# Performance work log

Measured on AMD Instinct MI355X. Metric: run time of the kernel, lower is better.

## Reference

```python
import jax, jax.numpy as jnp
import numpy as np

B, S, H = 2, 1024, 768
D, HID = 24, 96            # hdim_proj_dim, hdim_mlp_hidden
VIN, VHID = 3 * H, 2 * max(128, H // 2)  # concat_hadam -> 3H; out_hid = 768
ALPHA0 = 0.05              # init_gate_hdim


def setup_inputs() -> dict:
    key = jax.random.key(0)
    ks = jax.random.split(key, 10)
    sc = 0.02
    return {
        "H_j": jax.random.normal(ks[0], (B, S, H), jnp.float32),
        "H_i": jax.random.normal(ks[1], (B, S, H), jnp.float32),
        "attn_mask": jnp.ones((B, S), jnp.float32),
        "Wpj": jax.random.normal(ks[2], (H, D), jnp.float32) * sc,
        "Wpi": jax.random.normal(ks[3], (H, D), jnp.float32) * sc,
        "W1": jax.random.normal(ks[4], (4 * D, HID), jnp.float32) * sc,
        "b1": jnp.zeros((HID,), jnp.float32),
        "W2": jax.random.normal(ks[5], (HID, 1), jnp.float32) * sc,
        "b2": jnp.zeros((1,), jnp.float32),
        "Wv1": jax.random.normal(ks[6], (VIN, VHID), jnp.float32) * sc,
        "bv1": jnp.zeros((VHID,), jnp.float32),
        "Wv2": jax.random.normal(ks[7], (VHID, H), jnp.float32) * sc,
        "bv2": jnp.zeros((H,), jnp.float32),
        "alpha": jnp.float32(ALPHA0),
    }


def reference(H_j, H_i, attn_mask, Wpj, Wpi, W1, b1, W2, b2, Wv1, bv1, Wv2, bv2, alpha):
    # token projections: [B,S,D]
    Zj = H_j @ Wpj
    Zi = H_i @ Wpi
    # 4-term pair MLP, decomposed so the [B,S,S,4D] concat is never built:
    # cat([Zj_pair, Zi_pair, Zj*Zi, |Zj-Zi|]) @ W1 == sum of 4 partial products
    W1a, W1b, W1c, W1d = W1[:D], W1[D:2 * D], W1[2 * D:3 * D], W1[3 * D:]
    tj = Zj @ W1a                                   # [B,S,HID]
    ti = Zi @ W1b                                   # [B,S,HID]
    had = jnp.einsum('bsd,btd,dh->bsth', Zj, Zi, W1c)          # [B,S,S,HID]
    diff = jnp.abs(Zj[:, :, None, :] - Zi[:, None, :, :]) @ W1d  # [B,S,S,HID]
    h = jax.nn.relu(tj[:, :, None, :] + ti[:, None, :, :] + had + diff + b1)
    logits = (h @ W2)[..., 0] + b2[0]               # [B,S,S]
    # additive mask on key axis (torch: (1-mask)*finfo.min)
    logits = logits + (1.0 - attn_mask[:, None, :]) * jnp.finfo(logits.dtype).min
    probs = jax.nn.softmax(logits, axis=-1)
    ctx = jnp.einsum('bst,bth->bsh', probs, H_i)    # context over H_i
    # value fusion: concat_hadam -> [ctx, H_j, ctx*H_j]
    msg_in = jnp.concatenate([ctx, H_j, ctx * H_j], axis=-1)
    msg = jax.nn.relu(msg_in @ Wv1 + bv1) @ Wv2 + bv2
    return alpha * msg  # dropout is identity at eval
```

## Files before the change

kernel.cpp:

```cpp
#include <hip/hip_runtime.h>
#include <math.h>

#define BB   2
#define SS   1024
#define HH   768
#define DD   24
#define HIDD 96
#define VINN 2304
#define VHIDD 768
#define NRR  2048

typedef __attribute__((ext_vector_type(8))) short short8;
typedef __attribute__((ext_vector_type(4))) float floatx4;

static __device__ inline unsigned short f2bf(float x) {
    unsigned int u = __float_as_uint(x);
    u = (u + 0x7FFFu + ((u >> 16) & 1u)) >> 16;
    return (unsigned short)u;
}
static __device__ inline unsigned int pack2(float a, float b) {
    return (unsigned int)f2bf(a) | ((unsigned int)f2bf(b) << 16);
}

static __device__ inline void gl16(const unsigned short* g, unsigned short* l) {
    __builtin_amdgcn_global_load_lds(
        (const __attribute__((address_space(1))) unsigned int*)g,
        (__attribute__((address_space(3))) unsigned int*)l,
        16, 0, 0);
}

__global__ __launch_bounds__(256) void k_tconv(
    const float* __restrict__ in, unsigned short* __restrict__ out,
    int R, int C)
{
    size_t zoff = (size_t)blockIdx.z * R * C;
    in += zoff; out += zoff;
    __shared__ float tile[32][33];
    int r0 = blockIdx.y * 32, c0 = blockIdx.x * 32;
    int tc = threadIdx.x & 31, tr = threadIdx.x >> 5;
    #pragma unroll
    for (int i = 0; i < 4; ++i)
        tile[tr + i*8][tc] = in[(size_t)(r0 + tr + i*8)*C + c0 + tc];
    __syncthreads();
    #pragma unroll
    for (int i = 0; i < 4; ++i)
        out[(size_t)(c0 + tr + i*8)*R + r0 + tc] = f2bf(tile[tc][tr + i*8]);
}

__global__ __launch_bounds__(256) void k_zproj(
    const float* __restrict__ Hj, const float* __restrict__ Hi,
    const float* __restrict__ Wpj, const float* __restrict__ Wpi,
    unsigned* __restrict__ Zjp, unsigned* __restrict__ Zip)
{
    __shared__ __align__(16) unsigned short sA[64][72];
    __shared__ __align__(16) unsigned short sBT[32][72];
    int tid = threadIdx.x;
    int w = tid >> 6, lane = tid & 63;
    int quad = lane >> 4, col = lane & 15;

    int m0 = blockIdx.x * 64;
    bool isJ = (m0 < NRR);
    const float* src = isJ ? Hj : Hi;
    const float* Wp  = isJ ? Wpj : Wpi;
    unsigned* Zp     = isJ ? Zjp : Zip;
    int rowbase = isJ ? m0 : (m0 - NRR);

    floatx4 acc[2];
    acc[0] = (floatx4){0.f,0.f,0.f,0.f};
    acc[1] = (floatx4){0.f,0.f,0.f,0.f};

    for (int kb = 0; kb < HH; kb += 64) {
        #pragma unroll
        for (int i = 0; i < 4; ++i) {
            int f4 = tid + i*256;
            int r = f4 >> 4, c4 = f4 & 15;
            float4 v = *(const float4*)(src + (size_t)(rowbase + r)*HH + kb + c4*4);
            uint2 pkt; pkt.x = pack2(v.x, v.y); pkt.y = pack2(v.z, v.w);
            *(uint2*)&sA[r][c4*4] = pkt;
        }
        {
            const float* wsrc = Wp + (size_t)kb*DD;
            #pragma unroll
            for (int i = 0; i < 6; ++i) {
                int idx = tid + i*256;
                int k = idx / DD, n = idx % DD;
                sBT[n][k] = f2bf(wsrc[idx]);
            }
        }
        __syncthreads();
        #pragma unroll
        for (int kt = 0; kt < 2; ++kt) {
            short8 av = *(const short8*)&sA[w*16 + col][kt*32 + quad*8];
            #pragma unroll
            for (int nt = 0; nt < 2; ++nt) {
                short8 bv = *(const short8*)&sBT[nt*16 + col][kt*32 + quad*8];
                acc[nt] = __builtin_amdgcn_mfma_f32_16x16x32_bf16(av, bv, acc[nt], 0, 0, 0);
            }
        }
        __syncthreads();
    }
    #pragma unroll
    for (int nt = 0; nt < 2; ++nt) {
        #pragma unroll
        for (int r = 0; r < 4; ++r) {
            float v = acc[nt][r];
            float vn = __shfl_xor(v, 1, 64);
            int n = nt*16 + col;
            if (!(col & 1) && n < DD) {
                int m = w*16 + quad*4 + r;
                Zp[(size_t)(rowbase + m)*12 + (n >> 1)] = pack2(v, vn);
            }
        }
    }
}

#define LSTR 72
#define TC 128
__global__ __launch_bounds__(256) void k_attn(
    const unsigned* __restrict__ Zjp, const unsigned* __restrict__ Zip,
    const float* __restrict__ W1, const float* __restrict__ b1,
    const float* __restrict__ W2,
    const float* __restrict__ mask, unsigned short* __restrict__ probs)
{
    int row = blockIdx.x;
    int b = row >> 10;
    int tid = threadIdx.x;
    int lane = tid & 63, wv = tid >> 6;
    int quad = lane >> 4, col = lane & 15;

    __shared__ __align__(16) unsigned short sAB[2][TC*LSTR];
    __shared__ __align__(16) float sLog[SS];
    __shared__ unsigned sZjp[12];
    __shared__ float sW2[HIDD];
    __shared__ float sRed[4];

    if (tid < 12) sZjp[tid] = Zjp[(size_t)row*12 + tid];
    if (tid < HIDD) sW2[tid] = W2[tid];
    __syncthreads();

    if (tid < HIDD) {
        int h = tid;
        float zj[24];
        #pragma unroll
        for (int u = 0; u < 12; ++u) {
            unsigned z = sZjp[u];
            zj[2*u]   = __uint_as_float(z << 16);
            zj[2*u+1] = __uint_as_float(z & 0xffff0000u);
        }
        float tj = b1[h];
        #pragma unroll
        for (int d = 0; d < DD; ++d) tj = fmaf(zj[d], W1[d*HIDD + h], tj);
        unsigned short* rowp = &sAB[0][h*LSTR];
        #pragma unroll
        for (int d = 0; d < DD; ++d)
            rowp[d] = f2bf(fmaf(zj[d], W1[(48+d)*HIDD + h], W1[(24+d)*HIDD + h]));
        #pragma unroll
        for (int d = 0; d < DD; ++d)
            rowp[24+d] = f2bf(W1[(72+d)*HIDD + h]);
        rowp[48] = f2bf(tj);
        #pragma unroll
        for (int k = 49; k < 64; ++k) rowp[k] = 0;
    }
    __syncthreads();

    short8 bfr[6][2];
    #pragma unroll
    for (int nf = 0; nf < 6; ++nf)
        #pragma unroll
        for (int kt = 0; kt < 2; ++kt)
            bfr[nf][kt] = *(const short8*)&sAB[0][(nf*16 + col)*LSTR + kt*32 + quad*8];
    float4 w2q[6];
    #pragma unroll
    for (int nf = 0; nf < 6; ++nf)
        w2q[nf] = *(const float4*)&sW2[nf*16 + quad*4];
    __syncthreads();

    {
        int r = tid >> 1, bf = tid & 1;
        unsigned short* rowp = &sAB[bf][r*LSTR];
        uint4 w0; w0.x = 0x3F80u; w0.y = 0; w0.z = 0; w0.w = 0;
        *(uint4*)&rowp[48] = w0;
        uint4 zz; zz.x = 0; zz.y = 0; zz.z = 0; zz.w = 0;
        *(uint4*)&rowp[56] = zz;
    }

    int t_loc = tid >> 1, hh = tid & 1;
    const unsigned* zbase = Zip + (size_t)(b << 10) * 12;

    auto pack = [&](int chunk, int bf) {
        int t = chunk*TC + t_loc;
        const unsigned* zr = zbase + (size_t)t*12;
        unsigned short* rowp = &sAB[bf][t_loc*LSTR];
        uint4 first = *(const uint4*)(zr + hh*4);
        *(uint4*)&rowp[hh*8] = first;
        uint2 ext; ext.x = 0; ext.y = 0;
        if (hh) {
            uint4 second = *(const uint4*)(zr + 8);
            *(uint4*)&rowp[16] = second;
            unsigned myz[6] = {first.z, first.w, second.x, second.y, second.z, second.w};
            unsigned q[6];
            #pragma unroll
            for (int u = 0; u < 6; ++u) {
                unsigned za = sZjp[6 + u], zb = myz[u];
                float alo = __uint_as_float(za << 16);
                float ahi = __uint_as_float(za & 0xffff0000u);
                float blo = __uint_as_float(zb << 16);
                float bhi = __uint_as_float(zb & 0xffff0000u);
                unsigned dlo = __float_as_uint(fabsf(alo - blo)) + 0x8000u;
                unsigned dhi = __float_as_uint(fabsf(ahi - bhi)) + 0x8000u;
                q[u] = __builtin_amdgcn_perm(dhi, dlo, 0x07060302u);
            }
            #pragma unroll
            for (int j = 0; j < 3; ++j) {
                uint2 wq; wq.x = q[2*j]; wq.y = q[2*j+1];
                *(uint2*)&rowp[36 + 4*j] = wq;
            }
        } else {
            ext = *(const uint2*)(zr + 4);
            unsigned myz[6] = {first.x, first.y, first.z, first.w, ext.x, ext.y};
            unsigned q[6];
            #pragma unroll
            for (int u = 0; u < 6; ++u) {
                unsigned za = sZjp[u], zb = myz[u];
                float alo = __uint_as_float(za << 16);
                float ahi = __uint_as_float(za & 0xffff0000u);
                float blo = __uint_as_float(zb << 16);
                float bhi = __uint_as_float(zb & 0xffff0000u);
                unsigned dlo = __float_as_uint(fabsf(alo - blo)) + 0x8000u;
                unsigned dhi = __float_as_uint(fabsf(ahi - bhi)) + 0x8000u;
                q[u] = __builtin_amdgcn_perm(dhi, dlo, 0x07060302u);
            }
            #pragma unroll
            for (int j = 0; j < 3; ++j) {
                uint2 wq; wq.x = q[2*j]; wq.y = q[2*j+1];
                *(uint2*)&rowp[24 + 4*j] = wq;
            }
        }
    };

    pack(0, 0);
    __syncthreads();

    for (int chunk = 0; chunk < SS/TC; ++chunk) {
        int cur = chunk & 1;
        if (chunk + 1 < SS/TC) pack(chunk + 1, cur ^ 1);

        short8 av[2][2];
        #pragma unroll
        for (int tt = 0; tt < 2; ++tt) {
            int arow = (wv*2 + tt)*16 + col;
            av[tt][0] = *(const short8*)&sAB[cur][arow*LSTR + quad*8];
            av[tt][1] = *(const short8*)&sAB[cur][arow*LSTR + 32 + quad*8];
        }
        float s0 = 0.f, s1 = 0.f;
        #pragma unroll
        for (int hf = 0; hf < 6; ++hf) {
            floatx4 a0 = {0.f,0.f,0.f,0.f}, a1 = {0.f,0.f,0.f,0.f};
            a0 = __builtin_amdgcn_mfma_f32_16x16x32_bf16(bfr[hf][0], av[0][0], a0, 0, 0, 0);
            a0 = __builtin_amdgcn_mfma_f32_16x16x32_bf16(bfr[hf][1], av[0][1], a0, 0, 0, 0);
            a1 = __builtin_amdgcn_mfma_f32_16x16x32_bf16(bfr[hf][0], av[1][0], a1, 0, 0, 0);
            a1 = __builtin_amdgcn_mfma_f32_16x16x32_bf16(bfr[hf][1], av[1][1], a1, 0, 0, 0);
            float w2v[4] = {w2q[hf].x, w2q[hf].y, w2q[hf].z, w2q[hf].w};
            #pragma unroll
            for (int r = 0; r < 4; ++r) {
                s0 = fmaf(fmaxf(a0[r], 0.f), w2v[r], s0);
                s1 = fmaf(fmaxf(a1[r], 0.f), w2v[r], s1);
            }
        }
        s0 += __shfl_xor(s0, 16, 64);  s0 += __shfl_xor(s0, 32, 64);
        s1 += __shfl_xor(s1, 16, 64);  s1 += __shfl_xor(s1, 32, 64);
        if (lane < 16) {
            sLog[chunk*TC + (wv*2 + 0)*16 + lane] = s0;
            sLog[chunk*TC + (wv*2 + 1)*16 + lane] = s1;
        }
        __syncthreads();
    }

    float lv[4];
    #pragma unroll
    for (int i = 0; i < 4; ++i) {
        int t = tid + i*256;
        lv[i] = sLog[t] + (1.0f - mask[(size_t)(b<<10) + t]) * (-3.402823466e+38f);
    }
    float m = fmaxf(fmaxf(lv[0], lv[1]), fmaxf(lv[2], lv[3]));
    #pragma unroll
    for (int off = 32; off; off >>= 1) m = fmaxf(m, __shfl_down(m, off, 64));
    if (lane == 0) sRed[wv] = m;
    __syncthreads();
    float M = fmaxf(fmaxf(sRed[0], sRed[1]), fmaxf(sRed[2], sRed[3]));
    float e[4]; float ssum = 0.f;
    #pragma unroll
    for (int i = 0; i < 4; ++i) { e[i] = expf(lv[i] - M); ssum += e[i]; }
    #pragma unroll
    for (int off = 32; off; off >>= 1) ssum += __shfl_down(ssum, off, 64);
    __syncthreads();
    if (lane == 0) sRed[wv] = ssum;
    __syncthreads();
    float inv = 1.0f / (sRed[0] + sRed[1] + sRed[2] + sRed[3]);
    #pragma unroll
    for (int i = 0; i < 4; ++i)
        probs[(size_t)row*SS + tid + i*256] = f2bf(e[i] * inv);
}

__global__ __launch_bounds__(256) void k_mgemm_p(
    const unsigned short* __restrict__ A,
    const unsigned short* __restrict__ BT,
    float* __restrict__ P,
    int K, int bt_bstride)
{
    __shared__ __align__(16) unsigned short sA[64*64];
    __shared__ __align__(16) unsigned short sB[64*64];
    int tid = threadIdx.x;
    int w = tid >> 6, lane = tid & 63;
    int quad = lane >> 4, col = lane & 15;

    int n0 = blockIdx.x * 64, m0 = blockIdx.y * 64;
    int z = blockIdx.z;
    int kslice = K >> 1;
    int k0 = z * kslice;
    int nk = kslice >> 6;
    const unsigned short* Bb = BT + (size_t)(m0 >> 10) * bt_bstride;

    int srow = lane >> 3;
    int skc  = (lane & 7) * 8;

    floatx4 acc[4];
    #pragma unroll
    for (int nf = 0; nf < 4; ++nf) acc[nf] = (floatx4){0.f,0.f,0.f,0.f};

    for (int kb = 0; kb < nk; ++kb) {
        int kofs = k0 + kb*64;
        #pragma unroll
        for (int i = 0; i < 2; ++i) {
            int rbase = w*16 + i*8;
            gl16(A  + (size_t)(m0 + rbase + srow)*K + kofs + skc, &sA[rbase*64]);
            gl16(Bb + (size_t)(n0 + rbase + srow)*K + kofs + skc, &sB[rbase*64]);
        }
        __syncthreads();
        #pragma unroll
        for (int kt = 0; kt < 2; ++kt) {
            short8 av = *(const short8*)&sA[(w*16 + col)*64 + kt*32 + quad*8];
            #pragma unroll
            for (int nf = 0; nf < 4; ++nf) {
                short8 bv = *(const short8*)&sB[(nf*16 + col)*64 + kt*32 + quad*8];
                acc[nf] = __builtin_amdgcn_mfma_f32_16x16x32_bf16(av, bv, acc[nf], 0, 0, 0);
            }
        }
        __syncthreads();
    }

    float* Pz = P + (size_t)z*NRR*768;
    #pragma unroll
    for (int nf = 0; nf < 4; ++nf) {
        int n = n0 + nf*16 + col;
        #pragma unroll
        for (int r = 0; r < 4; ++r) {
            int m = w*16 + quad*4 + r;
            Pz[(size_t)(m0 + m)*768 + n] = acc[nf][r];
        }
    }
}

template<int MODE>
__global__ __launch_bounds__(256) void k_epi(
    const float* __restrict__ P,
    const float* __restrict__ bias,
    const float* __restrict__ Hj,
    const float* __restrict__ alpha_p,
    void* __restrict__ Cout)
{
    int idx = blockIdx.x*256 + threadIdx.x;
    int g = idx / 192, c = (idx % 192) * 4;
    float4 v0 = *(const float4*)(P + (size_t)g*768 + c);
    float4 v1 = *(const float4*)(P + (size_t)NRR*768 + (size_t)g*768 + c);
    float v[4] = {v0.x+v1.x, v0.y+v1.y, v0.z+v1.z, v0.w+v1.w};
    if (MODE == 0) {
        float4 h4 = *(const float4*)(Hj + (size_t)g*HH + c);
        float hj[4] = {h4.x, h4.y, h4.z, h4.w};
        unsigned short* msgin = (unsigned short*)Cout;
        uint2 wc, wh, wp;
        wc.x = pack2(v[0], v[1]);        wc.y = pack2(v[2], v[3]);
        wh.x = pack2(hj[0], hj[1]);      wh.y = pack2(hj[2], hj[3]);
        wp.x = pack2(v[0]*hj[0], v[1]*hj[1]);
        wp.y = pack2(v[2]*hj[2], v[3]*hj[3]);
        *(uint2*)&msgin[(size_t)g*VINN + c]        = wc;
        *(uint2*)&msgin[(size_t)g*VINN + HH + c]   = wh;
        *(uint2*)&msgin[(size_t)g*VINN + 2*HH + c] = wp;
    } else if (MODE == 1) {
        float4 b4 = *(const float4*)(bias + c);
        uint2 wy;
        wy.x = pack2(fmaxf(v[0]+b4.x, 0.f), fmaxf(v[1]+b4.y, 0.f));
        wy.y = pack2(fmaxf(v[2]+b4.z, 0.f), fmaxf(v[3]+b4.w, 0.f));
        *(uint2*)&((unsigned short*)Cout)[(size_t)g*VHIDD + c] = wy;
    } else {
        float a = alpha_p[0];
        float4 b4 = *(const float4*)(bias + c);
        float4 o;
        o.x = a*(v[0]+b4.x); o.y = a*(v[1]+b4.y);
        o.z = a*(v[2]+b4.z); o.w = a*(v[3]+b4.w);
        *(float4*)&((float*)Cout)[(size_t)g*HH + c] = o;
    }
}

extern "C" void kernel_launch(void* const* d_in, const int* in_sizes, int n_in,
                              void* d_out, int out_size, void* d_ws, size_t ws_size,
                              hipStream_t stream)
{
    const float* Hj   = (const float*)d_in[0];
    const float* Hi   = (const float*)d_in[1];
    const float* mask = (const float*)d_in[2];
    const float* Wpj  = (const float*)d_in[3];
    const float* Wpi  = (const float*)d_in[4];
    const float* W1   = (const float*)d_in[5];
    const float* b1   = (const float*)d_in[6];
    const float* W2   = (const float*)d_in[7];
    const float* Wv1  = (const float*)d_in[9];
    const float* bv1  = (const float*)d_in[10];
    const float* Wv2  = (const float*)d_in[11];
    const float* bv2  = (const float*)d_in[12];
    const float* alpha = (const float*)d_in[13];
    float* out = (float*)d_out;

    const int NR = NRR;
    char* p = (char*)d_ws;
    auto alloc = [&](size_t bytes) {
        char* r = p; p += (bytes + 255) & ~(size_t)255; return r;
    };
    unsigned* Zjp          = (unsigned*)alloc((size_t)NR*12*4);
    unsigned* Zip          = (unsigned*)alloc((size_t)NR*12*4);
    unsigned short* probsb = (unsigned short*)alloc((size_t)NR*SS*2);
    unsigned short* HiT    = (unsigned short*)alloc((size_t)BB*HH*SS*2);
    unsigned short* Wv1T   = (unsigned short*)alloc((size_t)VHIDD*VINN*2);
    unsigned short* Wv2T   = (unsigned short*)alloc((size_t)HH*VHIDD*2);
    unsigned short* msginb = (unsigned short*)alloc((size_t)NR*VINN*2);
    unsigned short* Y1b    = (unsigned short*)alloc((size_t)NR*VHIDD*2);
    float* Part            = (float*)alloc((size_t)2*NR*768*4);

    k_tconv<<<dim3(VHIDD/32, VINN/32, 1), 256, 0, stream>>>(Wv1, Wv1T, VINN, VHIDD);
    k_tconv<<<dim3(HH/32, VHIDD/32, 1), 256, 0, stream>>>(Wv2, Wv2T, VHIDD, HH);
    k_tconv<<<dim3(HH/32, SS/32, BB), 256, 0, stream>>>(Hi, HiT, SS, HH);
    k_zproj<<<2*NR/64, 256, 0, stream>>>(Hj, Hi, Wpj, Wpi, Zjp, Zip);
    k_attn<<<NR, 256, 0, stream>>>(Zjp, Zip, W1, b1, W2, mask, probsb);

    const int EPI_GRID = NR*192/256;

    k_mgemm_p<<<dim3(HH/64, NR/64, 2), 256, 0, stream>>>(
        probsb, HiT, Part, SS, HH*SS);
    k_epi<0><<<EPI_GRID, 256, 0, stream>>>(Part, nullptr, Hj, alpha, msginb);

    k_mgemm_p<<<dim3(VHIDD/64, NR/64, 2), 256, 0, stream>>>(
        msginb, Wv1T, Part, VINN, 0);
    k_epi<1><<<EPI_GRID, 256, 0, stream>>>(Part, bv1, nullptr, alpha, Y1b);

    k_mgemm_p<<<dim3(HH/64, NR/64, 2), 256, 0, stream>>>(
        Y1b, Wv2T, Part, VHIDD, 0);
    k_epi<2><<<EPI_GRID, 256, 0, stream>>>(Part, bv2, nullptr, alpha, out);
}
```

Before: 216.9 us.

## Merge prep kernels and fuse epilogues into non-split-K GEMMs

```diff
diff --git a/kernel.cpp b/kernel.cpp
--- a/kernel.cpp
+++ b/kernel.cpp
@@ -29,15 +29,97 @@
         16, 0, 0);
 }
 
-__global__ __launch_bounds__(256) void k_tconv(
-    const float* __restrict__ in, unsigned short* __restrict__ out,
-    int R, int C)
+__global__ __launch_bounds__(256) void k_prep(
+    const float* __restrict__ Hj, const float* __restrict__ Hi,
+    const float* __restrict__ Wpj, const float* __restrict__ Wpi,
+    const float* __restrict__ Wv1, const float* __restrict__ Wv2,
+    unsigned* __restrict__ Zjp, unsigned* __restrict__ Zip,
+    unsigned short* __restrict__ Wv1T, unsigned short* __restrict__ Wv2T,
+    unsigned short* __restrict__ HiT)
 {
-    size_t zoff = (size_t)blockIdx.z * R * C;
-    in += zoff; out += zoff;
+    __shared__ __align__(16) unsigned short sAz[64][72];
+    __shared__ __align__(16) unsigned short sBTz[32][72];
     __shared__ float tile[32][33];
-    int r0 = blockIdx.y * 32, c0 = blockIdx.x * 32;
-    int tc = threadIdx.x & 31, tr = threadIdx.x >> 5;
+    int bid = blockIdx.x;
+    int tid = threadIdx.x;
+
+    if (bid < 64) {
+        int w = tid >> 6, lane = tid & 63;
+        int quad = lane >> 4, col = lane & 15;
+        int m0 = bid * 64;
+        bool isJ = (m0 < NRR);
+        const float* src = isJ ? Hj : Hi;
+        const float* Wp  = isJ ? Wpj : Wpi;
+        unsigned* Zp     = isJ ? Zjp : Zip;
+        int rowbase = isJ ? m0 : (m0 - NRR);
+
+        floatx4 acc[2];
+        acc[0] = (floatx4){0.f,0.f,0.f,0.f};
+        acc[1] = (floatx4){0.f,0.f,0.f,0.f};
+
+        for (int kb = 0; kb < HH; kb += 64) {
+            #pragma unroll
+            for (int i = 0; i < 4; ++i) {
+                int f4 = tid + i*256;
+                int r = f4 >> 4, c4 = f4 & 15;
+                float4 v = *(const float4*)(src + (size_t)(rowbase + r)*HH + kb + c4*4);
+                uint2 pkt; pkt.x = pack2(v.x, v.y); pkt.y = pack2(v.z, v.w);
+                *(uint2*)&sAz[r][c4*4] = pkt;
+            }
+            {
+                const float* wsrc = Wp + (size_t)kb*DD;
+                #pragma unroll
+                for (int i = 0; i < 6; ++i) {
+                    int idx = tid + i*256;
+                    int k = idx / DD, n = idx % DD;
+                    sBTz[n][k] = f2bf(wsrc[idx]);
+                }
+            }
+            __syncthreads();
+            #pragma unroll
+            for (int kt = 0; kt < 2; ++kt) {
+                short8 av = *(const short8*)&sAz[w*16 + col][kt*32 + quad*8];
+                #pragma unroll
+                for (int nt = 0; nt < 2; ++nt) {
+                    short8 bv = *(const short8*)&sBTz[nt*16 + col][kt*32 + quad*8];
+                    acc[nt] = __builtin_amdgcn_mfma_f32_16x16x32_bf16(av, bv, acc[nt], 0, 0, 0);
+                }
+            }
+            __syncthreads();
+        }
+        #pragma unroll
+        for (int nt = 0; nt < 2; ++nt) {
+            #pragma unroll
+            for (int r = 0; r < 4; ++r) {
+                float v = acc[nt][r];
+                float vn = __shfl_xor(v, 1, 64);
+                int n = nt*16 + col;
+                if (!(col & 1) && n < DD) {
+                    int m = w*16 + quad*4 + r;
+                    Zp[(size_t)(rowbase + m)*12 + (n >> 1)] = pack2(v, vn);
+                }
+            }
+        }
+        return;
+    }
+
+    int b2 = bid - 64;
+    const float* in; unsigned short* out; int R, C, r0, c0;
+    if (b2 < 1728) {
+        in = Wv1; out = Wv1T; R = VINN; C = VHIDD;
+        c0 = (b2 % 24) * 32; r0 = (b2 / 24) * 32;
+    } else if (b2 < 2304) {
+        int t = b2 - 1728;
+        in = Wv2; out = Wv2T; R = VHIDD; C = HH;
+        c0 = (t % 24) * 32; r0 = (t / 24) * 32;
+    } else {
+        int t = b2 - 2304;
+        int z = t / 768; t %= 768;
+        in = Hi + (size_t)z*SS*HH; out = HiT + (size_t)z*HH*SS;
+        R = SS; C = HH;
+        c0 = (t % 24) * 32; r0 = (t / 24) * 32;
+    }
+    int tc = tid & 31, tr = tid >> 5;
     #pragma unroll
     for (int i = 0; i < 4; ++i)
         tile[tr + i*8][tc] = in[(size_t)(r0 + tr + i*8)*C + c0 + tc];
@@ -45,73 +127,6 @@
     #pragma unroll
     for (int i = 0; i < 4; ++i)
         out[(size_t)(c0 + tr + i*8)*R + r0 + tc] = f2bf(tile[tc][tr + i*8]);
-}
-
-__global__ __launch_bounds__(256) void k_zproj(
-    const float* __restrict__ Hj, const float* __restrict__ Hi,
-    const float* __restrict__ Wpj, const float* __restrict__ Wpi,
-    unsigned* __restrict__ Zjp, unsigned* __restrict__ Zip)
-{
-    __shared__ __align__(16) unsigned short sA[64][72];
-    __shared__ __align__(16) unsigned short sBT[32][72];
-    int tid = threadIdx.x;
-    int w = tid >> 6, lane = tid & 63;
-    int quad = lane >> 4, col = lane & 15;
-
-    int m0 = blockIdx.x * 64;
-    bool isJ = (m0 < NRR);
-    const float* src = isJ ? Hj : Hi;
-    const float* Wp  = isJ ? Wpj : Wpi;
-    unsigned* Zp     = isJ ? Zjp : Zip;
-    int rowbase = isJ ? m0 : (m0 - NRR);
-
-    floatx4 acc[2];
-    acc[0] = (floatx4){0.f,0.f,0.f,0.f};
-    acc[1] = (floatx4){0.f,0.f,0.f,0.f};
-
-    for (int kb = 0; kb < HH; kb += 64) {
-        #pragma unroll
-        for (int i = 0; i < 4; ++i) {
-            int f4 = tid + i*256;
-            int r = f4 >> 4, c4 = f4 & 15;
-            float4 v = *(const float4*)(src + (size_t)(rowbase + r)*HH + kb + c4*4);
-            uint2 pkt; pkt.x = pack2(v.x, v.y); pkt.y = pack2(v.z, v.w);
-            *(uint2*)&sA[r][c4*4] = pkt;
-        }
-        {
-            const float* wsrc = Wp + (size_t)kb*DD;
-            #pragma unroll
-            for (int i = 0; i < 6; ++i) {
-                int idx = tid + i*256;
-                int k = idx / DD, n = idx % DD;
-                sBT[n][k] = f2bf(wsrc[idx]);
-            }
-        }
-        __syncthreads();
-        #pragma unroll
-        for (int kt = 0; kt < 2; ++kt) {
-            short8 av = *(const short8*)&sA[w*16 + col][kt*32 + quad*8];
-            #pragma unroll
-            for (int nt = 0; nt < 2; ++nt) {
-                short8 bv = *(const short8*)&sBT[nt*16 + col][kt*32 + quad*8];
-                acc[nt] = __builtin_amdgcn_mfma_f32_16x16x32_bf16(av, bv, acc[nt], 0, 0, 0);
-            }
-        }
-        __syncthreads();
-    }
-    #pragma unroll
-    for (int nt = 0; nt < 2; ++nt) {
-        #pragma unroll
-        for (int r = 0; r < 4; ++r) {
-            float v = acc[nt][r];
-            float vn = __shfl_xor(v, 1, 64);
-            int n = nt*16 + col;
-            if (!(col & 1) && n < DD) {
-                int m = w*16 + quad*4 + r;
-                Zp[(size_t)(rowbase + m)*12 + (n >> 1)] = pack2(v, vn);
-            }
-        }
-    }
 }
 
 #define LSTR 72
@@ -362,44 +377,86 @@
 }
 
 template<int MODE>
-__global__ __launch_bounds__(256) void k_epi(
-    const float* __restrict__ P,
+__global__ __launch_bounds__(256) void k_mgemm_nf(
+    const unsigned short* __restrict__ A,
+    const unsigned short* __restrict__ BT,
     const float* __restrict__ bias,
     const float* __restrict__ Hj,
     const float* __restrict__ alpha_p,
-    void* __restrict__ Cout)
+    void* __restrict__ Cout,
+    int K, int bt_bstride)
+{
+    __shared__ __align__(16) unsigned short sA[64*64];
+    __shared__ __align__(16) unsigned short sB[32*64];
+    int tid = threadIdx.x;
+    int w = tid >> 6, lane = tid & 63;
+    int quad = lane >> 4, col = lane & 15;
+
+    int n0 = blockIdx.x * 32, m0 = blockIdx.y * 64;
+    int nk = K >> 6;
+    const unsigned short* Bb = BT + (size_t)(m0 >> 10) * bt_bstride;
+
+    int srow = lane >> 3;
+    int skc  = (lane & 7) * 8;
+
+    floatx4 acc[2];
+    acc[0] = (floatx4){0.f,0.f,0.f,0.f};
+    acc[1] = (floatx4){0.f,0.f,0.f,0.f};
+
+    for (int kb = 0; kb < nk; ++kb) {
+        int kofs = kb*64;
+        gl16(A  + (size_t)(m0 + w*16     + srow)*K + kofs + skc, &sA[(w*16)*64]);
+        gl16(A  + (size_t)(m0 + w*16 + 8 + srow)*K + kofs + skc, &sA[(w*16 + 8)*64]);
+        gl16(Bb + (size_t)(n0 + w*8      + srow)*K + kofs + skc, &sB[(w*8)*64]);
+        __syncthreads();
+        #pragma unroll
+        for (int kt = 0; kt < 2; ++kt) {
+            short8 av = *(const short8*)&sA[(w*16 + col)*64 + kt*32 + quad*8];
+            #pragma unroll
+            for (int nf = 0; nf < 2; ++nf) {
+                short8 bv = *(const short8*)&sB[(nf*16 + col)*64 + kt*32 + quad*8];
+                acc[nf] = __builtin_amdgcn_mfma_f32_16x16x32_bf16(av, bv, acc[nf], 0, 0, 0);
+            }
+        }
+        __syncthreads();
+    }
+
+    float alpha = (MODE == 2) ? alpha_p[0] : 1.0f;
+    #pragma unroll
+    for (int nf = 0; nf < 2; ++nf) {
+        int n = n0 + nf*16 + col;
+        #pragma unroll
+        for (int r = 0; r < 4; ++r) {
+            int m = w*16 + quad*4 + r;
+            size_t g = (size_t)(m0 + m);
+            float v = acc[nf][r];
+            if (MODE == 0) {
+                float hj = Hj[g*HH + n];
+                unsigned short* msgin = (unsigned short*)Cout;
+                msgin[g*VINN + n]        = f2bf(v);
+                msgin[g*VINN + HH + n]   = f2bf(hj);
+                msgin[g*VINN + 2*HH + n] = f2bf(v*hj);
+            } else {
+                ((float*)Cout)[g*HH + n] = alpha*(v + bias[n]);
+            }
+        }
+    }
+}
+
+__global__ __launch_bounds__(256) void k_epi1(
+    const float* __restrict__ P,
+    const float* __restrict__ bias,
+    unsigned short* __restrict__ Y1)
 {
     int idx = blockIdx.x*256 + threadIdx.x;
     int g = idx / 192, c = (idx % 192) * 4;
     float4 v0 = *(const float4*)(P + (size_t)g*768 + c);
     float4 v1 = *(const float4*)(P + (size_t)NRR*768 + (size_t)g*768 + c);
-    float v[4] = {v0.x+v1.x, v0.y+v1.y, v0.z+v1.z, v0.w+v1.w};
-    if (MODE == 0) {
-        float4 h4 = *(const float4*)(Hj + (size_t)g*HH + c);
-        float hj[4] = {h4.x, h4.y, h4.z, h4.w};
-        unsigned short* msgin = (unsigned short*)Cout;
-        uint2 wc, wh, wp;
-        wc.x = pack2(v[0], v[1]);        wc.y = pack2(v[2], v[3]);
-        wh.x = pack2(hj[0], hj[1]);      wh.y = pack2(hj[2], hj[3]);
-        wp.x = pack2(v[0]*hj[0], v[1]*hj[1]);
-        wp.y = pack2(v[2]*hj[2], v[3]*hj[3]);
-        *(uint2*)&msgin[(size_t)g*VINN + c]        = wc;
-        *(uint2*)&msgin[(size_t)g*VINN + HH + c]   = wh;
-        *(uint2*)&msgin[(size_t)g*VINN + 2*HH + c] = wp;
-    } else if (MODE == 1) {
-        float4 b4 = *(const float4*)(bias + c);
-        uint2 wy;
-        wy.x = pack2(fmaxf(v[0]+b4.x, 0.f), fmaxf(v[1]+b4.y, 0.f));
-        wy.y = pack2(fmaxf(v[2]+b4.z, 0.f), fmaxf(v[3]+b4.w, 0.f));
-        *(uint2*)&((unsigned short*)Cout)[(size_t)g*VHIDD + c] = wy;
-    } else {
-        float a = alpha_p[0];
-        float4 b4 = *(const float4*)(bias + c);
-        float4 o;
-        o.x = a*(v[0]+b4.x); o.y = a*(v[1]+b4.y);
-        o.z = a*(v[2]+b4.z); o.w = a*(v[3]+b4.w);
-        *(float4*)&((float*)Cout)[(size_t)g*HH + c] = o;
-    }
+    float4 b4 = *(const float4*)(bias + c);
+    uint2 wy;
+    wy.x = pack2(fmaxf(v0.x+v1.x+b4.x, 0.f), fmaxf(v0.y+v1.y+b4.y, 0.f));
+    wy.y = pack2(fmaxf(v0.z+v1.z+b4.z, 0.f), fmaxf(v0.w+v1.w+b4.w, 0.f));
+    *(uint2*)&Y1[(size_t)g*VHIDD + c] = wy;
 }
 
 extern "C" void kernel_launch(void* const* d_in, const int* in_sizes, int n_in,
@@ -436,23 +493,18 @@
     unsigned short* Y1b    = (unsigned short*)alloc((size_t)NR*VHIDD*2);
     float* Part            = (float*)alloc((size_t)2*NR*768*4);
 
-    k_tconv<<<dim3(VHIDD/32, VINN/32, 1), 256, 0, stream>>>(Wv1, Wv1T, VINN, VHIDD);
-    k_tconv<<<dim3(HH/32, VHIDD/32, 1), 256, 0, stream>>>(Wv2, Wv2T, VHIDD, HH);
-    k_tconv<<<dim3(HH/32, SS/32, BB), 256, 0, stream>>>(Hi, HiT, SS, HH);
-    k_zproj<<<2*NR/64, 256, 0, stream>>>(Hj, Hi, Wpj, Wpi, Zjp, Zip);
+    k_prep<<<64 + 1728 + 576 + 1536, 256, 0, stream>>>(
+        Hj, Hi, Wpj, Wpi, Wv1, Wv2, Zjp, Zip, Wv1T, Wv2T, HiT);
+
     k_attn<<<NR, 256, 0, stream>>>(Zjp, Zip, W1, b1, W2, mask, probsb);
 
-    const int EPI_GRID = NR*192/256;
-
-    k_mgemm_p<<<dim3(HH/64, NR/64, 2), 256, 0, stream>>>(
-        probsb, HiT, Part, SS, HH*SS);
-    k_epi<0><<<EPI_GRID, 256, 0, stream>>>(Part, nullptr, Hj, alpha, msginb);
+    k_mgemm_nf<0><<<dim3(HH/32, NR/64), 256, 0, stream>>>(
+        probsb, HiT, nullptr, Hj, alpha, msginb, SS, HH*SS);
 
     k_mgemm_p<<<dim3(VHIDD/64, NR/64, 2), 256, 0, stream>>>(
         msginb, Wv1T, Part, VINN, 0);
-    k_epi<1><<<EPI_GRID, 256, 0, stream>>>(Part, bv1, nullptr, alpha, Y1b);
-
-    k_mgemm_p<<<dim3(HH/64, NR/64, 2), 256, 0, stream>>>(
-        Y1b, Wv2T, Part, VHIDD, 0);
-    k_epi<2><<<EPI_GRID, 256, 0, stream>>>(Part, bv2, nullptr, alpha, out);
-}
+    k_epi1<<<NR*192/256, 256, 0, stream>>>(Part, bv1, Y1b);
+
+    k_mgemm_nf<2><<<dim3(HH/32, NR/64), 256, 0, stream>>>(
+        Y1b, Wv2T, bv2, nullptr, alpha, out, VHIDD, 0);
+}
```

Measured after the change: 207.5 us. -4.3%, faster.
